# Kernel tuning notes

Measured on AMD Instinct MI355X. Metric: run time of the kernel, lower is better.

Reference implementation:

```python
import jax, jax.numpy as jnp
import numpy as np

N, E, D, H = 100000, 1000000, 64, 64  # nodes, edges, input_dim, output_dim
EPS = 1e-5


def _lin(k, fi, fo):
    return jax.random.normal(k, (fi, fo), jnp.float32) / np.sqrt(fi)


def setup_inputs() -> dict:
    key = jax.random.key(0)
    ks = jax.random.split(key, 8)
    x = jax.random.normal(ks[0], (N, D), jnp.float32)
    e = jax.random.uniform(ks[1], (E,), jnp.float32)
    edge_index = jax.random.randint(ks[2], (2, E), 0, N, dtype=jnp.int32)
    return {
        "x": x,
        "e": e,
        "edge_index": edge_index,
        "W1": _lin(ks[3], 2 * D, H), "b1": jnp.zeros((H,), jnp.float32),
        "g1": jnp.ones((H,), jnp.float32), "be1": jnp.zeros((H,), jnp.float32),
        "W2": _lin(ks[4], H, H), "b2": jnp.zeros((H,), jnp.float32),
        "g2": jnp.ones((H,), jnp.float32), "be2": jnp.zeros((H,), jnp.float32),
        "W3": _lin(ks[5], H, H), "b3": jnp.zeros((H,), jnp.float32),
    }


def _layer_norm(h, g, b):
    mu = jnp.mean(h, axis=-1, keepdims=True)
    var = jnp.mean(jnp.square(h - mu), axis=-1, keepdims=True)
    return (h - mu) * jax.lax.rsqrt(var + EPS) * g + b


def reference(x, e, edge_index, W1, b1, g1, be1, W2, b2, g2, be2, W3, b3):
    start, end = edge_index[0], edge_index[1]
    we = e[:, None]  # [E,1]
    # edge-weighted gather-multiply-scatter_add, both directions
    mi = jax.ops.segment_sum(we * x[start], end, num_segments=N) \
       + jax.ops.segment_sum(we * x[end], start, num_segments=N)  # [N,D]
    h = jnp.concatenate([mi, x], axis=1)  # [N,2D]
    h = jnp.tanh(_layer_norm(h @ W1 + b1, g1, be1))
    h = jnp.tanh(_layer_norm(h @ W2 + b2, g2, be2))
    return h @ W3 + b3  # [N,H]
```

## Files before the change

### kernel.cpp

```cpp
#include <hip/hip_runtime.h>

typedef unsigned int u32;
typedef int   v4i __attribute__((ext_vector_type(4)));
typedef float v4f __attribute__((ext_vector_type(4)));

#define NMAX 100000
#define EMAX 1000000
#define CAP 64
#define NSHMAX 12500

__device__ __align__(16) float g_mi[NMAX * 64];
__device__ int g_deg[8 * NSHMAX];
__device__ __align__(16) u32 g_adj[(size_t)8 * NSHMAX * CAP];

__global__ __launch_bounds__(256) void fill_sharded(
    const int* __restrict__ src, const int* __restrict__ dst,
    const float* __restrict__ ew, int E, int NSH, int nchunk)
{
    int group = blockIdx.x & 7;
    int chunk = blockIdx.x >> 3;
    int stride = nchunk * 256 * 4;
    for (int e0 = (chunk * 256 + threadIdx.x) * 4; e0 < E; e0 += stride) {
        if (e0 + 3 < E) {
            v4i s4 = __builtin_nontemporal_load((const v4i*)&src[e0]);
            v4i t4 = __builtin_nontemporal_load((const v4i*)&dst[e0]);
            v4f w4 = __builtin_nontemporal_load((const v4f*)&ew[e0]);
            #pragma unroll
            for (int j = 0; j < 4; j++) {
                int s = s4[j], t = t4[j];
                float w = w4[j];
                int w15 = (int)(w * 32768.f + 0.5f);
                if (w15 > 32767) w15 = 32767;
                if ((s & 7) == group) {
                    int idx = group * NSH + (s >> 3);
                    int p = atomicAdd(&g_deg[idx], 1);
                    if (p < CAP) g_adj[(size_t)idx * CAP + p] = ((u32)t << 15) | (u32)w15;
                }
                if ((t & 7) == group) {
                    int idx = group * NSH + (t >> 3);
                    int q = atomicAdd(&g_deg[idx], 1);
                    if (q < CAP) g_adj[(size_t)idx * CAP + q] = ((u32)s << 15) | (u32)w15;
                }
            }
        } else {
            for (int e = e0; e < E; e++) {
                int s = src[e], t = dst[e];
                float w = ew[e];
                int w15 = (int)(w * 32768.f + 0.5f);
                if (w15 > 32767) w15 = 32767;
                if ((s & 7) == group) {
                    int idx = group * NSH + (s >> 3);
                    int p = atomicAdd(&g_deg[idx], 1);
                    if (p < CAP) g_adj[(size_t)idx * CAP + p] = ((u32)t << 15) | (u32)w15;
                }
                if ((t & 7) == group) {
                    int idx = group * NSH + (t >> 3);
                    int q = atomicAdd(&g_deg[idx], 1);
                    if (q < CAP) g_adj[(size_t)idx * CAP + q] = ((u32)s << 15) | (u32)w15;
                }
            }
        }
    }
}

__global__ __launch_bounds__(256) void gather4(const float* __restrict__ x,
                                               int N, int NSH) {
    int wid  = (blockIdx.x * 256 + threadIdx.x) >> 6;
    int lane = threadIdx.x & 63;
    int sub  = lane >> 4;
    int q    = lane & 15;
    int node = wid * 4 + sub;
    if (wid * 4 >= N) return;
    bool nvalid = node < N;
    int nodec = nvalid ? node : N - 1;
    int idx = (nodec & 7) * NSH + (nodec >> 3);
    int cnt = nvalid ? g_deg[idx] : 0;
    if (nvalid && q == 0) g_deg[idx] = 0;
    if (cnt > CAP) cnt = CAP;
    const u32* row = g_adj + (size_t)idx * CAP;

    int mc = cnt;
    mc = max(mc, __shfl_xor(mc, 16));
    mc = max(mc, __shfl_xor(mc, 32));

    int sgbase = sub << 4;
    v4f acc = {0.f, 0.f, 0.f, 0.f};

    for (int j0 = 0; j0 < mc; j0 += 16) {
        u32 ec = row[j0 + q];
        #pragma unroll
        for (int u = 0; u < 16; u++) {
            int j = j0 + u;
            u32 e = __shfl(ec, sgbase + u);
            bool val = (j < cnt);
            int nb   = val ? (int)(e >> 15) : nodec;
            float w  = val ? (float)(e & 0x7FFFu) * (1.f / 32768.f) : 0.f;
            v4f xv = *(const v4f*)&x[(size_t)nb * 64 + (q << 2)];
            acc[0] = fmaf(w, xv[0], acc[0]);
            acc[1] = fmaf(w, xv[1], acc[1]);
            acc[2] = fmaf(w, xv[2], acc[2]);
            acc[3] = fmaf(w, xv[3], acc[3]);
        }
    }
    if (nvalid) *(v4f*)&g_mi[(size_t)node * 64 + (q << 2)] = acc;
}

#define HS 68
#define SWF(f) ((((f) >> 2) & 7) << 2)

#define GEMM_PASS(WP) do {                                              \
    _Pragma("unroll 2")                                                 \
    for (int k = 0; k < 64; k++) {                                      \
        float a = ht[k * HS + (lane ^ SWF(k))];                         \
        const float* wp = (WP) + k * 64 + c0;                           \
        _Pragma("unroll")                                               \
        for (int c = 0; c < 16; c++) acc[c] = fmaf(a, wp[c], acc[c]);   \
    } } while (0)

__global__ __launch_bounds__(256, 8) void mlp(
    const float* __restrict__ x,
    const float* __restrict__ W1, const float* __restrict__ B1,
    const float* __restrict__ G1, const float* __restrict__ E1,
    const float* __restrict__ W2, const float* __restrict__ B2,
    const float* __restrict__ G2, const float* __restrict__ E2,
    const float* __restrict__ W3, const float* __restrict__ B3,
    float* __restrict__ out, int N)
{
    __shared__ float ht[64 * HS];
    __shared__ float lnb[4 * 64];

    int tid  = threadIdx.x;
    int lane = tid & 63;
    int c0   = __builtin_amdgcn_readfirstlane(tid >> 6) * 16;
    int n0 = blockIdx.x * 64;
    int nodes = N - n0; if (nodes > 64) nodes = 64;

    if (tid < 64) {
        lnb[tid]       = G1[tid];
        lnb[64 + tid]  = E1[tid];
        lnb[128 + tid] = G2[tid];
        lnb[192 + tid] = E2[tid];
    }

    float acc[16];
    #pragma unroll
    for (int c = 0; c < 16; c++) acc[c] = B1[c0 + c];

    #pragma unroll
    for (int it = 0; it < 4; it++) {
        int idx = tid + it * 256;
        int nd = idx >> 4, f4 = (idx & 15) * 4;
        v4f v = {0.f, 0.f, 0.f, 0.f};
        if (nd < nodes) v = *(const v4f*)&g_mi[(size_t)(n0 + nd) * 64 + f4];
        ht[(f4 + 0) * HS + (nd ^ SWF(f4 + 0))] = v[0];
        ht[(f4 + 1) * HS + (nd ^ SWF(f4 + 1))] = v[1];
        ht[(f4 + 2) * HS + (nd ^ SWF(f4 + 2))] = v[2];
        ht[(f4 + 3) * HS + (nd ^ SWF(f4 + 3))] = v[3];
    }
    __syncthreads();
    GEMM_PASS(W1);
    __syncthreads();

    #pragma unroll
    for (int it = 0; it < 4; it++) {
        int idx = tid + it * 256;
        int nd = idx >> 4, f4 = (idx & 15) * 4;
        v4f v = {0.f, 0.f, 0.f, 0.f};
        if (nd < nodes) v = *(const v4f*)&x[(size_t)(n0 + nd) * 64 + f4];
        ht[(f4 + 0) * HS + (nd ^ SWF(f4 + 0))] = v[0];
        ht[(f4 + 1) * HS + (nd ^ SWF(f4 + 1))] = v[1];
        ht[(f4 + 2) * HS + (nd ^ SWF(f4 + 2))] = v[2];
        ht[(f4 + 3) * HS + (nd ^ SWF(f4 + 3))] = v[3];
    }
    __syncthreads();
    GEMM_PASS(W1 + 64 * 64);
    __syncthreads();

    #pragma unroll
    for (int c = 0; c < 16; c++)
        ht[(c0 + c) * HS + (lane ^ SWF(c0 + c))] = acc[c];
    __syncthreads();

    if (tid < 64) {
        float mu = 0.f;
        for (int j = 0; j < 64; j++) mu += ht[j * HS + (tid ^ SWF(j))];
        mu *= (1.f / 64.f);
        float var = 0.f;
        for (int j = 0; j < 64; j++) { float d = ht[j * HS + (tid ^ SWF(j))] - mu; var += d * d; }
        var *= (1.f / 64.f);
        float rs = rsqrtf(var + 1e-5f);
        for (int j = 0; j < 64; j++) {
            float v = (ht[j * HS + (tid ^ SWF(j))] - mu) * rs * lnb[j] + lnb[64 + j];
            float ex = __expf(2.f * v);
            ht[j * HS + (tid ^ SWF(j))] = 1.f - 2.f / (ex + 1.f);
        }
    }
    __syncthreads();

    #pragma unroll
    for (int c = 0; c < 16; c++) acc[c] = B2[c0 + c];
    GEMM_PASS(W2);
    __syncthreads();
    #pragma unroll
    for (int c = 0; c < 16; c++)
        ht[(c0 + c) * HS + (lane ^ SWF(c0 + c))] = acc[c];
    __syncthreads();

    if (tid < 64) {
        float mu = 0.f;
        for (int j = 0; j < 64; j++) mu += ht[j * HS + (tid ^ SWF(j))];
        mu *= (1.f / 64.f);
        float var = 0.f;
        for (int j = 0; j < 64; j++) { float d = ht[j * HS + (tid ^ SWF(j))] - mu; var += d * d; }
        var *= (1.f / 64.f);
        float rs = rsqrtf(var + 1e-5f);
        for (int j = 0; j < 64; j++) {
            float v = (ht[j * HS + (tid ^ SWF(j))] - mu) * rs * lnb[128 + j] + lnb[192 + j];
            float ex = __expf(2.f * v);
            ht[j * HS + (tid ^ SWF(j))] = 1.f - 2.f / (ex + 1.f);
        }
    }
    __syncthreads();

    #pragma unroll
    for (int c = 0; c < 16; c++) acc[c] = B3[c0 + c];
    GEMM_PASS(W3);
    __syncthreads();
    #pragma unroll
    for (int c = 0; c < 16; c++)
        ht[(c0 + c) * HS + (lane ^ SWF(c0 + c))] = acc[c];
    __syncthreads();

    #pragma unroll
    for (int it = 0; it < 4; it++) {
        int idx = tid + it * 256;
        int nd = idx >> 4, f4 = (idx & 15) * 4;
        if (nd < nodes) {
            v4f v = { ht[(f4 + 0) * HS + (nd ^ SWF(f4 + 0))],
                      ht[(f4 + 1) * HS + (nd ^ SWF(f4 + 1))],
                      ht[(f4 + 2) * HS + (nd ^ SWF(f4 + 2))],
                      ht[(f4 + 3) * HS + (nd ^ SWF(f4 + 3))] };
            *(v4f*)&out[(size_t)(n0 + nd) * 64 + f4] = v;
        }
    }
}

extern "C" void kernel_launch(void* const* d_in, const int* in_sizes, int n_in,
                              void* d_out, int out_size, void* d_ws, size_t ws_size,
                              hipStream_t stream) {
    const float* x  = (const float*)d_in[0];
    const float* e  = (const float*)d_in[1];
    const int* ei   = (const int*)d_in[2];
    const float* W1 = (const float*)d_in[3];
    const float* b1 = (const float*)d_in[4];
    const float* g1 = (const float*)d_in[5];
    const float* be1= (const float*)d_in[6];
    const float* W2 = (const float*)d_in[7];
    const float* b2 = (const float*)d_in[8];
    const float* g2 = (const float*)d_in[9];
    const float* be2= (const float*)d_in[10];
    const float* W3 = (const float*)d_in[11];
    const float* b3 = (const float*)d_in[12];

    int N = in_sizes[0] / 64;
    int E = in_sizes[1];
    int NSH = (N + 7) / 8;

    int nchunk = 256;
    fill_sharded<<<8 * nchunk, 256, 0, stream>>>(ei, ei + E, e, E, NSH, nchunk);

    gather4<<<(N + 15) / 16, 256, 0, stream>>>(x, N, NSH);

    mlp<<<(N + 63) / 64, 256, 0, stream>>>(
        x, W1, b1, g1, be1, W2, b2, g2, be2, W3, b3, (float*)d_out, N);
}
```

Before: 333.2 us.

## Partition half-edges by shard before filling adjacency, vectorize MLP weight loads

Replaces the fill kernel, in which every one of 8 shard groups re-read the full edge list, with two stages. A partition kernel reads each edge once and uses block-local histograms plus global cursors to bucket packed half-edges into per-shard slices. A second kernel then scatters them into the adjacency lists. This removes the eightfold rereading of the edge arrays at the cost of an extra kernel launch, 8 MB of intermediate writes and reads, and global cursor atomics. Separately, the MLP GEMM inner loop now loads weights as float4 vectors, and c0 no longer goes through readfirstlane, which may move the weight loads off scalar loads.

```diff
diff --git a/kernel.cpp b/kernel.cpp
--- a/kernel.cpp
+++ b/kernel.cpp
@@ -1,6 +1,7 @@
 #include <hip/hip_runtime.h>
 
 typedef unsigned int u32;
+typedef unsigned long long u64;
 typedef int   v4i __attribute__((ext_vector_type(4)));
 typedef float v4f __attribute__((ext_vector_type(4)));
 
@@ -8,63 +9,91 @@
 #define EMAX 1000000
 #define CAP 64
 #define NSHMAX 12500
+#define SLICE 262144
 
 __device__ __align__(16) float g_mi[NMAX * 64];
 __device__ int g_deg[8 * NSHMAX];
+__device__ int g_cur[8];
 __device__ __align__(16) u32 g_adj[(size_t)8 * NSHMAX * CAP];
-
-__global__ __launch_bounds__(256) void fill_sharded(
+__device__ __align__(16) u64 g_he[(size_t)8 * SLICE];
+
+__global__ __launch_bounds__(256) void partition_he(
     const int* __restrict__ src, const int* __restrict__ dst,
-    const float* __restrict__ ew, int E, int NSH, int nchunk)
+    const float* __restrict__ ew, int E)
 {
-    int group = blockIdx.x & 7;
-    int chunk = blockIdx.x >> 3;
-    int stride = nchunk * 256 * 4;
-    for (int e0 = (chunk * 256 + threadIdx.x) * 4; e0 < E; e0 += stride) {
-        if (e0 + 3 < E) {
-            v4i s4 = __builtin_nontemporal_load((const v4i*)&src[e0]);
-            v4i t4 = __builtin_nontemporal_load((const v4i*)&dst[e0]);
-            v4f w4 = __builtin_nontemporal_load((const v4f*)&ew[e0]);
-            #pragma unroll
-            for (int j = 0; j < 4; j++) {
-                int s = s4[j], t = t4[j];
-                float w = w4[j];
-                int w15 = (int)(w * 32768.f + 0.5f);
-                if (w15 > 32767) w15 = 32767;
-                if ((s & 7) == group) {
-                    int idx = group * NSH + (s >> 3);
-                    int p = atomicAdd(&g_deg[idx], 1);
-                    if (p < CAP) g_adj[(size_t)idx * CAP + p] = ((u32)t << 15) | (u32)w15;
-                }
-                if ((t & 7) == group) {
-                    int idx = group * NSH + (t >> 3);
-                    int q = atomicAdd(&g_deg[idx], 1);
-                    if (q < CAP) g_adj[(size_t)idx * CAP + q] = ((u32)s << 15) | (u32)w15;
-                }
-            }
-        } else {
-            for (int e = e0; e < E; e++) {
-                int s = src[e], t = dst[e];
-                float w = ew[e];
-                int w15 = (int)(w * 32768.f + 0.5f);
-                if (w15 > 32767) w15 = 32767;
-                if ((s & 7) == group) {
-                    int idx = group * NSH + (s >> 3);
-                    int p = atomicAdd(&g_deg[idx], 1);
-                    if (p < CAP) g_adj[(size_t)idx * CAP + p] = ((u32)t << 15) | (u32)w15;
-                }
-                if ((t & 7) == group) {
-                    int idx = group * NSH + (t >> 3);
-                    int q = atomicAdd(&g_deg[idx], 1);
-                    if (q < CAP) g_adj[(size_t)idx * CAP + q] = ((u32)s << 15) | (u32)w15;
-                }
-            }
-        }
+    __shared__ int hist[8], gbase[8];
+    int tid = threadIdx.x;
+    int base = blockIdx.x * 1024;
+    if (base >= E) return;
+    if (tid < 8) hist[tid] = 0;
+    __syncthreads();
+
+    int e0 = base + tid * 4;
+    int sv[4], tv[4]; float wv[4];
+    int rs[4] = {0,0,0,0}, rt[4] = {0,0,0,0};
+    int nval = E - e0; if (nval < 0) nval = 0; if (nval > 4) nval = 4;
+    if (nval == 4) {
+        v4i s4 = __builtin_nontemporal_load((const v4i*)&src[e0]);
+        v4i t4 = __builtin_nontemporal_load((const v4i*)&dst[e0]);
+        v4f w4 = __builtin_nontemporal_load((const v4f*)&ew[e0]);
+        #pragma unroll
+        for (int j = 0; j < 4; j++) { sv[j] = s4[j]; tv[j] = t4[j]; wv[j] = w4[j]; }
+    } else {
+        #pragma unroll
+        for (int j = 0; j < 4; j++) {
+            if (j < nval) { sv[j] = src[e0+j]; tv[j] = dst[e0+j]; wv[j] = ew[e0+j]; }
+            else          { sv[j] = 0; tv[j] = 0; wv[j] = 0.f; }
+        }
+    }
+    #pragma unroll
+    for (int j = 0; j < 4; j++) {
+        if (j < nval) {
+            rs[j] = atomicAdd(&hist[sv[j] & 7], 1);
+            rt[j] = atomicAdd(&hist[tv[j] & 7], 1);
+        }
+    }
+    __syncthreads();
+    if (tid < 8) gbase[tid] = atomicAdd(&g_cur[tid], hist[tid]);
+    __syncthreads();
+    #pragma unroll
+    for (int j = 0; j < 4; j++) {
+        if (j < nval) {
+            int s = sv[j], t = tv[j];
+            int w15 = (int)(wv[j] * 32768.f + 0.5f);
+            if (w15 > 32767) w15 = 32767;
+            int gs = s & 7, gt = t & 7;
+            int ps = gbase[gs] + rs[j];
+            int pt = gbase[gt] + rt[j];
+            if (ps < SLICE)
+                __builtin_nontemporal_store(
+                    ((u64)(u32)s << 32) | ((u32)t << 15) | (u32)w15,
+                    &g_he[(size_t)gs * SLICE + ps]);
+            if (pt < SLICE)
+                __builtin_nontemporal_store(
+                    ((u64)(u32)t << 32) | ((u32)s << 15) | (u32)w15,
+                    &g_he[(size_t)gt * SLICE + pt]);
+        }
+    }
+}
+
+__global__ __launch_bounds__(256) void fill_part(int NSH) {
+    int g = blockIdx.x & 7;
+    int cnt = g_cur[g]; if (cnt > SLICE) cnt = SLICE;
+    const u64* he = g_he + (size_t)g * SLICE;
+    int stride = (gridDim.x >> 3) * 256;
+    for (int i = (blockIdx.x >> 3) * 256 + threadIdx.x; i < cnt; i += stride) {
+        u64 p = __builtin_nontemporal_load(&he[i]);
+        int owner = (int)(p >> 32);
+        u32 ent = (u32)p;
+        int idx = g * NSH + (owner >> 3);
+        int q = atomicAdd(&g_deg[idx], 1);
+        if (q < CAP) g_adj[(size_t)idx * CAP + q] = ent;
     }
 }
 
 __global__ __launch_bounds__(256) void gather4(const float* __restrict__ x,
                                                int N, int NSH) {
+    if (blockIdx.x == 0 && threadIdx.x < 8) g_cur[threadIdx.x] = 0;
     int wid  = (blockIdx.x * 256 + threadIdx.x) >> 6;
     int lane = threadIdx.x & 63;
     int sub  = lane >> 4;
@@ -112,9 +141,16 @@
     _Pragma("unroll 2")                                                 \
     for (int k = 0; k < 64; k++) {                                      \
         float a = ht[k * HS + (lane ^ SWF(k))];                         \
-        const float* wp = (WP) + k * 64 + c0;                           \
+        const v4f* wp = (const v4f*)((WP) + k * 64 + c0);               \
+        v4f w0 = wp[0], w1 = wp[1], w2 = wp[2], w3 = wp[3];             \
         _Pragma("unroll")                                               \
-        for (int c = 0; c < 16; c++) acc[c] = fmaf(a, wp[c], acc[c]);   \
+        for (int c = 0; c < 4; c++) acc[c]      = fmaf(a, w0[c], acc[c]);      \
+        _Pragma("unroll")                                               \
+        for (int c = 0; c < 4; c++) acc[4 + c]  = fmaf(a, w1[c], acc[4 + c]);  \
+        _Pragma("unroll")                                               \
+        for (int c = 0; c < 4; c++) acc[8 + c]  = fmaf(a, w2[c], acc[8 + c]);  \
+        _Pragma("unroll")                                               \
+        for (int c = 0; c < 4; c++) acc[12 + c] = fmaf(a, w3[c], acc[12 + c]); \
     } } while (0)
 
 __global__ __launch_bounds__(256, 8) void mlp(
@@ -131,7 +167,7 @@
 
     int tid  = threadIdx.x;
     int lane = tid & 63;
-    int c0   = __builtin_amdgcn_readfirstlane(tid >> 6) * 16;
+    int c0   = (tid >> 6) * 16;
     int n0 = blockIdx.x * 64;
     int nodes = N - n0; if (nodes > 64) nodes = 64;
 
@@ -266,8 +302,10 @@
     int E = in_sizes[1];
     int NSH = (N + 7) / 8;
 
-    int nchunk = 256;
-    fill_sharded<<<8 * nchunk, 256, 0, stream>>>(ei, ei + E, e, E, NSH, nchunk);
+    int nb1 = (E + 1023) / 1024;
+    partition_he<<<nb1, 256, 0, stream>>>(ei, ei + E, e, E);
+
+    fill_part<<<2048, 256, 0, stream>>>(NSH);
 
     gather4<<<(N + 15) / 16, 256, 0, stream>>>(x, N, NSH);
 
```

New measurement: 508.4 us. +52.6%, slower.
